# Performance work log

Hardware: AMD Instinct MI355X
Metric: run time of the kernel (lower is better)

The kernel has to match this reference:

```python
import jax, jax.numpy as jnp
import numpy as np

HID = 256
NCLASS = 5
DEPTH = 11          # complete binary tree, N = 2**DEPTH - 1 nodes
BATCH = 128
N_NODES = 2 ** DEPTH - 1


def setup_inputs() -> dict:
    key = jax.random.key(0)
    ks = jax.random.split(key, 16)
    scale = 0.1
    def mat(k, shape):
        return scale * jax.random.normal(k, shape, dtype=jnp.float32)
    inp = {
        "x": jax.random.normal(ks[0], (BATCH, N_NODES, HID), dtype=jnp.float32),
        "W_i": mat(ks[1], (HID, HID)),
        "U_i": mat(ks[2], (2, HID, HID)),
        "b_i": jnp.zeros((HID,), jnp.float32),
        "W_f": mat(ks[3], (HID, HID)),
        "U_f": mat(ks[4], (2, 2, HID, HID)),
        "b_f": jnp.zeros((HID,), jnp.float32),
        "W_o": mat(ks[5], (HID, HID)),
        "U_o": mat(ks[6], (2, HID, HID)),
        "b_o": jnp.zeros((HID,), jnp.float32),
        "W_u": mat(ks[7], (HID, HID)),
        "U_u": mat(ks[8], (2, HID, HID)),
        "b_u": jnp.zeros((HID,), jnp.float32),
        "W_s": mat(ks[9], (NCLASS, HID)),
        "b_s": jnp.zeros((NCLASS,), jnp.float32),
    }
    return inp


def _mv(W, v):
    # W: [h,h] (or [c,h]), v: [B,M,h] -> [B,M,h_out]; matches U.mul(h).sum(dim=1)
    return jnp.einsum('ij,bmj->bmi', W, v)


def _tree_lstm(x, W_i, U_i, b_i, W_f, U_f, b_f, W_o, U_o, b_o, W_u, U_u, b_u):
    B, N, h = x.shape
    D = int(round(np.log2(N + 1)))
    h_all = jnp.zeros_like(x)   # init_tree: node_h = zeros
    c_all = jnp.zeros_like(x)   # init_tree: cell   = zeros
    for lvl in range(D - 1, -1, -1):  # bottom-up over tree levels
        s = 2 ** lvl - 1
        e = 2 ** (lvl + 1) - 1
        M = e - s
        x_lvl = x[:, s:e]                      # [B,M,h]
        if lvl == D - 1:  # leaves: children states are the zero-initialized ones
            hL = hR = cL = cR = jnp.zeros((B, M, h), x.dtype)
        else:
            # children of node i=s+j are at e+2j (left) and e+2j+1 (right)
            hc = h_all[:, e:e + 2 * M].reshape(B, M, 2, h)
            cc = c_all[:, e:e + 2 * M].reshape(B, M, 2, h)
            hL, hR = hc[:, :, 0], hc[:, :, 1]
            cL, cR = cc[:, :, 0], cc[:, :, 1]
        i_g = jax.nn.sigmoid(_mv(W_i, x_lvl) + _mv(U_i[0], hL) + _mv(U_i[1], hR) + b_i)
        o_g = jax.nn.sigmoid(_mv(W_o, x_lvl) + _mv(U_o[0], hL) + _mv(U_o[1], hR) + b_o)
        u_g = jnp.tanh(_mv(W_u, x_lvl) + _mv(U_u[0], hL) + _mv(U_u[1], hR) + b_u)
        Wfx = _mv(W_f, x_lvl)
        f0 = jax.nn.sigmoid(Wfx + _mv(U_f[0, 0], hL) + _mv(U_f[0, 1], hR) + b_f)
        f1 = jax.nn.sigmoid(Wfx + _mv(U_f[1, 0], hL) + _mv(U_f[1, 1], hR) + b_f)
        c_lvl = i_g * u_g + f0 * cL + f1 * cR
        h_lvl = o_g * jnp.tanh(c_lvl)
        h_all = h_all.at[:, s:e].set(h_lvl)
        c_all = c_all.at[:, s:e].set(c_lvl)
    return h_all


def reference(x, W_i, U_i, b_i, W_f, U_f, b_f, W_o, U_o, b_o, W_u, U_u, b_u, W_s, b_s):
    h_all = _tree_lstm(x, W_i, U_i, b_i, W_f, U_f, b_f, W_o, U_o, b_o, W_u, U_u, b_u)
    # PredictUpTree (dropout omitted for the deterministic reference):
    logits = jnp.einsum('ch,bnh->bnc', W_s, h_all) + b_s   # [B,N,Nclass]
    return jax.nn.softmax(logits, axis=-1)
```

## Files before the change

kernel.cpp:

```cpp
#include <hip/hip_runtime.h>
#include <math.h>

#define HID 256
#define NCLASS 5
#define DEPTH 11
#define NB 128
#define NN 2047

typedef __attribute__((ext_vector_type(8))) short bf16x8_t;
typedef __attribute__((ext_vector_type(4))) float f32x4_t;

__device__ __forceinline__ float bf2f(unsigned short u) {
    return __uint_as_float(((unsigned)u) << 16);
}
__device__ __forceinline__ unsigned short f2bf(float f) {
    unsigned x = __float_as_uint(f);
    unsigned r = (x + 0x7fff + ((x >> 16) & 1)) >> 16;
    return (unsigned short)r;
}
__device__ __forceinline__ float sigmoidf_(float x) {
    return __fdividef(1.0f, 1.0f + __expf(-x));
}
__device__ __forceinline__ float tanhf_(float x) {
    return 1.0f - __fdividef(2.0f, __expf(2.0f * x) + 1.0f);
}
__device__ __forceinline__ void gl_lds16(const void* g, void* l) {
    __builtin_amdgcn_global_load_lds(
        (const __attribute__((address_space(1))) unsigned int*)g,
        (__attribute__((address_space(3))) unsigned int*)l,
        16, 0, 0);
}

__global__ __launch_bounds__(256)
void prep_wcat(const float* __restrict__ W_i, const float* __restrict__ U_i,
               const float* __restrict__ W_f, const float* __restrict__ U_f,
               const float* __restrict__ W_o, const float* __restrict__ U_o,
               const float* __restrict__ W_u, const float* __restrict__ U_u,
               unsigned short* __restrict__ Wcat)
{
    int idx = blockIdx.x * 256 + threadIdx.x;
    int k = idx % 768;
    int n = idx / 768;
    int g = n >> 8;
    int ch = n & 255;
    int seg = k >> 8;
    int kk = k & 255;
    float v;
    if (seg == 0) {
        const float* W = (g == 0) ? W_i : (g == 1) ? W_o : (g == 2) ? W_u : W_f;
        v = W[ch * 256 + kk];
    } else {
        int side = seg - 1;
        if (g == 0)      v = U_i[(side * 256 + ch) * 256 + kk];
        else if (g == 1) v = U_o[(side * 256 + ch) * 256 + kk];
        else if (g == 2) v = U_u[(side * 256 + ch) * 256 + kk];
        else             v = U_f[(((g - 3) * 2 + side) * 256 + ch) * 256 + kk];
    }
    Wcat[(size_t)n * 768 + k] = f2bf(v);
}

__global__ __launch_bounds__(256)
void cast_x_kernel(const float* __restrict__ x, unsigned short* __restrict__ xb)
{
    size_t i = ((size_t)blockIdx.x * 256 + threadIdx.x) * 8;
    float4 a = *(const float4*)(x + i);
    float4 b = *(const float4*)(x + i + 4);
    unsigned short o[8] = {f2bf(a.x), f2bf(a.y), f2bf(a.z), f2bf(a.w),
                           f2bf(b.x), f2bf(b.y), f2bf(b.z), f2bf(b.w)};
    *(uint4*)(xb + i) = *(uint4*)o;
}

template<int NG, int NK, bool LEAF>
__global__ __launch_bounds__(512, 4)
void level_gemm(const unsigned short* __restrict__ xb,
                const unsigned short* __restrict__ hA,
                const unsigned short* __restrict__ Wcat,
                const float* __restrict__ c_child,
                const float* __restrict__ b_i, const float* __restrict__ b_o,
                const float* __restrict__ b_u, const float* __restrict__ b_f,
                float* __restrict__ c_out,
                unsigned short* __restrict__ hA_parent,
                unsigned short* __restrict__ h_all,
                int lgM)
{
    constexpr int NT = NG * 4;
    constexpr int BOFF = 8192;
    constexpr int BUFSZ = BOFF + NT * 1024;
    __shared__ __align__(16) char smem[2 * BUFSZ];

    const int tid  = threadIdx.x;
    const int w    = tid >> 6, lane = tid & 63;
    const int quad = lane >> 4, p = lane & 15;
    const int rh = w & 1, cq = w >> 1;
    const int chblk = blockIdx.x;
    const int R0 = blockIdx.y * 128;
    const int M = 1 << lgM, s = M - 1;

    const int arow = R0 + w * 16 + p;
    const int ab = arow >> lgM, am = arow & (M - 1);
    const unsigned short* a_x = xb + ((size_t)ab * NN + s + am) * 256 + quad * 8;
    const unsigned short* a_h = LEAF ? (const unsigned short*)nullptr
                                     : hA + (size_t)arow * 512 + quad * 8;
    const int nbt = LEAF ? (w < 4 ? 2 : 1) : (w < 4 ? 3 : 2);
    const int t0  = LEAF ? (w < 4 ? w * 2 : 8 + (w - 4))
                         : (w < 4 ? w * 3 : 12 + (w - 4) * 2);
    const unsigned short* bsrc[3];
    #pragma unroll
    for (int j = 0; j < 3; ++j) {
        int t = t0 + ((j < nbt) ? j : 0);
        int n = (t >> 2) * 256 + chblk * 64 + (t & 3) * 16 + p;
        bsrc[j] = Wcat + (size_t)n * 768 + quad * 8;
    }

    f32x4_t acc[4][NG];
    #pragma unroll
    for (int mi = 0; mi < 4; ++mi)
        #pragma unroll
        for (int j = 0; j < NG; ++j)
            acc[mi][j] = (f32x4_t){0.f, 0.f, 0.f, 0.f};

    {
        gl_lds16(a_x, smem + w * 1024);
        #pragma unroll
        for (int j = 0; j < 3; ++j)
            if (j < nbt) gl_lds16(bsrc[j], smem + BOFF + (t0 + j) * 1024);
    }
    __syncthreads();

    for (int step = 0; step < NK; ++step) {
        char* bufc = smem + (size_t)(step & 1) * BUFSZ;
        if (step + 1 < NK) {
            char* bufn = smem + (size_t)((step + 1) & 1) * BUFSZ;
            const int k0 = (step + 1) * 32;
            const unsigned short* asrc = (LEAF || k0 < 256) ? (a_x + k0) : (a_h + (k0 - 256));
            gl_lds16(asrc, bufn + w * 1024);
            #pragma unroll
            for (int j = 0; j < 3; ++j)
                if (j < nbt) gl_lds16(bsrc[j] + k0, bufn + BOFF + (t0 + j) * 1024);
        }
        __builtin_amdgcn_sched_barrier(0);

        bf16x8_t af[4];
        #pragma unroll
        for (int mi = 0; mi < 4; ++mi)
            af[mi] = *(const bf16x8_t*)(bufc + ((rh * 4 + mi) * 64 + lane) * 16);
        __builtin_amdgcn_s_setprio(1);
        #pragma unroll
        for (int j = 0; j < NG; ++j) {
            bf16x8_t bfr = *(const bf16x8_t*)(bufc + BOFF + ((j * 4 + cq) * 64 + lane) * 16);
            #pragma unroll
            for (int mi = 0; mi < 4; ++mi)
                acc[mi][j] = __builtin_amdgcn_mfma_f32_16x16x32_bf16(af[mi], bfr, acc[mi][j], 0, 0, 0);
        }
        __builtin_amdgcn_s_setprio(0);
        __syncthreads();
    }

    const int gch = chblk * 64 + cq * 16 + p;
    const float bi = b_i[gch], bo = b_o[gch], bu = b_u[gch];
    const float bfv = LEAF ? 0.f : b_f[gch];

    #pragma unroll
    for (int mi = 0; mi < 4; ++mi) {
        const int rowq = R0 + rh * 64 + mi * 16 + quad * 4;
        #pragma unroll
        for (int reg = 0; reg < 4; ++reg) {
            const int grow = rowq + reg;
            const int b = grow >> lgM, m = grow & (M - 1);
            float ig = sigmoidf_(acc[mi][0][reg] + bi);
            float og = sigmoidf_(acc[mi][1][reg] + bo);
            float ug = tanhf_(acc[mi][2][reg] + bu);
            float c;
            if (LEAF) {
                c = ig * ug;
            } else {
                const float* crow = c_child + ((size_t)b * (M << 1) + 2 * m) * 256 + gch;
                float f0 = sigmoidf_(acc[mi][3][reg] + bfv);
                float f1 = sigmoidf_(acc[mi][4][reg] + bfv);
                c = fmaf(f0, crow[0], fmaf(f1, crow[256], ig * ug));
            }
            float h = og * tanhf_(c);
            c_out[(size_t)grow * 256 + gch] = c;
            unsigned short hb = f2bf(h);
            h_all[((size_t)b * NN + s + m) * 256 + gch] = hb;
            if (hA_parent)
                hA_parent[((size_t)b * (M >> 1) + (m >> 1)) * 512 + (m & 1) * 256 + gch] = hb;
        }
    }
}

__global__ __launch_bounds__(256)
void softmax_kernel(const unsigned short* __restrict__ h_all,
                    const float* __restrict__ W_s, const float* __restrict__ b_s,
                    float* __restrict__ out)
{
    __shared__ float Ws[5 * 256];
    int tid = threadIdx.x;
    for (int i = tid; i < 1280; i += 256) Ws[i] = W_s[i];
    __syncthreads();

    int r = tid >> 3, q = tid & 7;
    size_t row = (size_t)blockIdx.x * 32 + r;
    const unsigned short* hp = h_all + row * 256 + q * 32;

    float p0 = 0.f, p1 = 0.f, p2 = 0.f, p3 = 0.f, p4 = 0.f;
    #pragma unroll
    for (int kk = 0; kk < 32; kk += 8) {
        uint4 raw = *(const uint4*)(hp + kk);
        unsigned short hu[8];
        *(uint4*)hu = raw;
        #pragma unroll
        for (int e = 0; e < 8; ++e) {
            float hvv = bf2f(hu[e]);
            int k = q * 32 + kk + e;
            p0 = fmaf(Ws[k],        hvv, p0);
            p1 = fmaf(Ws[256 + k],  hvv, p1);
            p2 = fmaf(Ws[512 + k],  hvv, p2);
            p3 = fmaf(Ws[768 + k],  hvv, p3);
            p4 = fmaf(Ws[1024 + k], hvv, p4);
        }
    }
    #pragma unroll
    for (int off = 4; off; off >>= 1) {
        p0 += __shfl_down(p0, off, 8);
        p1 += __shfl_down(p1, off, 8);
        p2 += __shfl_down(p2, off, 8);
        p3 += __shfl_down(p3, off, 8);
        p4 += __shfl_down(p4, off, 8);
    }
    if (q == 0) {
        float l0 = p0 + b_s[0], l1 = p1 + b_s[1], l2 = p2 + b_s[2];
        float l3 = p3 + b_s[3], l4 = p4 + b_s[4];
        float mx = fmaxf(fmaxf(fmaxf(l0, l1), fmaxf(l2, l3)), l4);
        float e0 = __expf(l0 - mx), e1 = __expf(l1 - mx), e2 = __expf(l2 - mx);
        float e3 = __expf(l3 - mx), e4 = __expf(l4 - mx);
        float inv = 1.0f / (e0 + e1 + e2 + e3 + e4);
        float* orow = out + row * NCLASS;
        orow[0] = e0 * inv;
        orow[1] = e1 * inv;
        orow[2] = e2 * inv;
        orow[3] = e3 * inv;
        orow[4] = e4 * inv;
    }
}

extern "C" void kernel_launch(void* const* d_in, const int* in_sizes, int n_in,
                              void* d_out, int out_size, void* d_ws, size_t ws_size,
                              hipStream_t stream) {
    const float* x   = (const float*)d_in[0];
    const float* W_i = (const float*)d_in[1];
    const float* U_i = (const float*)d_in[2];
    const float* b_i = (const float*)d_in[3];
    const float* W_f = (const float*)d_in[4];
    const float* U_f = (const float*)d_in[5];
    const float* b_f = (const float*)d_in[6];
    const float* W_o = (const float*)d_in[7];
    const float* U_o = (const float*)d_in[8];
    const float* b_o = (const float*)d_in[9];
    const float* W_u = (const float*)d_in[10];
    const float* U_u = (const float*)d_in[11];
    const float* b_u = (const float*)d_in[12];
    const float* W_s = (const float*)d_in[13];
    const float* b_s = (const float*)d_in[14];
    float* out = (float*)d_out;

    char* p = (char*)d_ws;
    unsigned short* Wcat  = (unsigned short*)p; p += 2097152;
    unsigned short* xb    = (unsigned short*)p; p += 134152192;
    unsigned short* h_all = (unsigned short*)p; p += 134152192;
    unsigned short* hA0   = (unsigned short*)p; p += 33554432;
    unsigned short* hA1   = (unsigned short*)p; p += 67108864;
    float* cb0 = (float*)p; p += 134217728;
    float* cb1 = (float*)p; p += 67108864;

    prep_wcat<<<3840, 256, 0, stream>>>(W_i, U_i, W_f, U_f, W_o, U_o, W_u, U_u, Wcat);
    cast_x_kernel<<<32752, 256, 0, stream>>>(x, xb);

    for (int lvl = DEPTH - 1; lvl >= 0; --lvl) {
        dim3 grid(4, 1 << lvl);
        float* c_o        = (lvl & 1) ? cb1 : cb0;
        const float* c_ch = ((lvl + 1) & 1) ? cb1 : cb0;
        const unsigned short* hA_this = (lvl & 1) ? hA1 : hA0;
        unsigned short* hA_par = (lvl > 0) ? (((lvl - 1) & 1) ? hA1 : hA0) : nullptr;

        if (lvl == DEPTH - 1) {
            level_gemm<3, 8, true><<<grid, 512, 0, stream>>>(
                xb, nullptr, Wcat, nullptr, b_i, b_o, b_u, b_f,
                c_o, hA_par, h_all, lvl);
        } else {
            level_gemm<5, 24, false><<<grid, 512, 0, stream>>>(
                xb, hA_this, Wcat, c_ch, b_i, b_o, b_u, b_f,
                c_o, hA_par, h_all, lvl);
        }
    }

    softmax_kernel<<<8188, 256, 0, stream>>>(h_all, W_s, b_s, out);
}
```

Before: 1.299 ms.

## Replace LDS-staged GEMM with direct global-to-register double buffering and block swizzle

```diff
diff --git a/kernel.cpp b/kernel.cpp
--- a/kernel.cpp
+++ b/kernel.cpp
@@ -23,12 +23,6 @@
 }
 __device__ __forceinline__ float tanhf_(float x) {
     return 1.0f - __fdividef(2.0f, __expf(2.0f * x) + 1.0f);
-}
-__device__ __forceinline__ void gl_lds16(const void* g, void* l) {
-    __builtin_amdgcn_global_load_lds(
-        (const __attribute__((address_space(1))) unsigned int*)g,
-        (__attribute__((address_space(3))) unsigned int*)l,
-        16, 0, 0);
 }
 
 __global__ __launch_bounds__(256)
@@ -71,7 +65,7 @@
 }
 
 template<int NG, int NK, bool LEAF>
-__global__ __launch_bounds__(512, 4)
+__global__ __launch_bounds__(512, LEAF ? 3 : 2)
 void level_gemm(const unsigned short* __restrict__ xb,
                 const unsigned short* __restrict__ hA,
                 const unsigned short* __restrict__ Wcat,
@@ -81,35 +75,43 @@
                 float* __restrict__ c_out,
                 unsigned short* __restrict__ hA_parent,
                 unsigned short* __restrict__ h_all,
-                int lgM)
+                int lgM, int nrb)
 {
-    constexpr int NT = NG * 4;
-    constexpr int BOFF = 8192;
-    constexpr int BUFSZ = BOFF + NT * 1024;
-    __shared__ __align__(16) char smem[2 * BUFSZ];
-
     const int tid  = threadIdx.x;
-    const int w    = tid >> 6, lane = tid & 63;
+    const int lane = tid & 63;
+    const int w    = tid >> 6;
     const int quad = lane >> 4, p = lane & 15;
     const int rh = w & 1, cq = w >> 1;
-    const int chblk = blockIdx.x;
-    const int R0 = blockIdx.y * 128;
+
+    int chblk, rb;
+    {
+        int bid = blockIdx.x;
+        if ((nrb & 7) == 0) {
+            int x = bid & 7, sl = bid >> 3;
+            chblk = sl & 3;
+            rb = x + 8 * (sl >> 2);
+        } else {
+            chblk = bid & 3;
+            rb = bid >> 2;
+        }
+    }
+    const int R0 = rb * 128;
     const int M = 1 << lgM, s = M - 1;
 
-    const int arow = R0 + w * 16 + p;
-    const int ab = arow >> lgM, am = arow & (M - 1);
-    const unsigned short* a_x = xb + ((size_t)ab * NN + s + am) * 256 + quad * 8;
-    const unsigned short* a_h = LEAF ? (const unsigned short*)nullptr
-                                     : hA + (size_t)arow * 512 + quad * 8;
-    const int nbt = LEAF ? (w < 4 ? 2 : 1) : (w < 4 ? 3 : 2);
-    const int t0  = LEAF ? (w < 4 ? w * 2 : 8 + (w - 4))
-                         : (w < 4 ? w * 3 : 12 + (w - 4) * 2);
-    const unsigned short* bsrc[3];
-    #pragma unroll
-    for (int j = 0; j < 3; ++j) {
-        int t = t0 + ((j < nbt) ? j : 0);
-        int n = (t >> 2) * 256 + chblk * 64 + (t & 3) * 16 + p;
-        bsrc[j] = Wcat + (size_t)n * 768 + quad * 8;
+    const unsigned short* ax[4];
+    const unsigned short* ah[4];
+    #pragma unroll
+    for (int mi = 0; mi < 4; ++mi) {
+        const int arow = R0 + (rh * 4 + mi) * 16 + p;
+        const int ab = arow >> lgM, am = arow & (M - 1);
+        ax[mi] = xb + ((size_t)ab * NN + s + am) * 256 + quad * 8;
+        ah[mi] = LEAF ? ax[mi] : hA + (size_t)arow * 512 + quad * 8;
+    }
+    const unsigned short* bb[NG];
+    #pragma unroll
+    for (int j = 0; j < NG; ++j) {
+        int n = j * 256 + chblk * 64 + cq * 16 + p;
+        bb[j] = Wcat + (size_t)n * 768 + quad * 8;
     }
 
     f32x4_t acc[4][NG];
@@ -119,42 +121,41 @@
         for (int j = 0; j < NG; ++j)
             acc[mi][j] = (f32x4_t){0.f, 0.f, 0.f, 0.f};
 
-    {
-        gl_lds16(a_x, smem + w * 1024);
-        #pragma unroll
-        for (int j = 0; j < 3; ++j)
-            if (j < nbt) gl_lds16(bsrc[j], smem + BOFF + (t0 + j) * 1024);
-    }
-    __syncthreads();
-
-    for (int step = 0; step < NK; ++step) {
-        char* bufc = smem + (size_t)(step & 1) * BUFSZ;
-        if (step + 1 < NK) {
-            char* bufn = smem + (size_t)((step + 1) & 1) * BUFSZ;
-            const int k0 = (step + 1) * 32;
-            const unsigned short* asrc = (LEAF || k0 < 256) ? (a_x + k0) : (a_h + (k0 - 256));
-            gl_lds16(asrc, bufn + w * 1024);
-            #pragma unroll
-            for (int j = 0; j < 3; ++j)
-                if (j < nbt) gl_lds16(bsrc[j] + k0, bufn + BOFF + (t0 + j) * 1024);
-        }
-        __builtin_amdgcn_sched_barrier(0);
-
-        bf16x8_t af[4];
-        #pragma unroll
-        for (int mi = 0; mi < 4; ++mi)
-            af[mi] = *(const bf16x8_t*)(bufc + ((rh * 4 + mi) * 64 + lane) * 16);
-        __builtin_amdgcn_s_setprio(1);
-        #pragma unroll
-        for (int j = 0; j < NG; ++j) {
-            bf16x8_t bfr = *(const bf16x8_t*)(bufc + BOFF + ((j * 4 + cq) * 64 + lane) * 16);
-            #pragma unroll
-            for (int mi = 0; mi < 4; ++mi)
-                acc[mi][j] = __builtin_amdgcn_mfma_f32_16x16x32_bf16(af[mi], bfr, acc[mi][j], 0, 0, 0);
-        }
-        __builtin_amdgcn_s_setprio(0);
-        __syncthreads();
-    }
+    bf16x8_t fa0[4], fa1[4];
+    bf16x8_t fb0[NG], fb1[NG];
+
+    #define LOAD_A(k0, fa)                                                        \
+        _Pragma("unroll")                                                         \
+        for (int mi = 0; mi < 4; ++mi) {                                          \
+            const unsigned short* srcA = (LEAF || (k0) < 256) ? (ax[mi] + (k0))   \
+                                                  : (ah[mi] + ((k0) - 256));      \
+            fa[mi] = *(const bf16x8_t*)srcA;                                      \
+        }
+    #define LOAD_B(k0, fb)                                                        \
+        _Pragma("unroll")                                                         \
+        for (int j = 0; j < NG; ++j)                                              \
+            fb[j] = *(const bf16x8_t*)(bb[j] + (k0));
+    #define COMPUTE(fa, fb)                                                       \
+        _Pragma("unroll")                                                         \
+        for (int j = 0; j < NG; ++j)                                              \
+            _Pragma("unroll")                                                     \
+            for (int mi = 0; mi < 4; ++mi)                                        \
+                acc[mi][j] = __builtin_amdgcn_mfma_f32_16x16x32_bf16(             \
+                    fa[mi], fb[j], acc[mi][j], 0, 0, 0);
+
+    LOAD_A(0, fa0); LOAD_B(0, fb0);
+    LOAD_A(32, fa1); LOAD_B(32, fb1);
+
+    #pragma unroll
+    for (int st = 0; st < NK; st += 2) {
+        COMPUTE(fa0, fb0);
+        if (st + 2 < NK) { LOAD_A((st + 2) * 32, fa0); LOAD_B((st + 2) * 32, fb0); }
+        COMPUTE(fa1, fb1);
+        if (st + 3 < NK) { LOAD_A((st + 3) * 32, fa1); LOAD_B((st + 3) * 32, fb1); }
+    }
+    #undef LOAD_A
+    #undef LOAD_B
+    #undef COMPUTE
 
     const int gch = chblk * 64 + cq * 16 + p;
     const float bi = b_i[gch], bo = b_o[gch], bu = b_u[gch];
@@ -163,6 +164,17 @@
     #pragma unroll
     for (int mi = 0; mi < 4; ++mi) {
         const int rowq = R0 + rh * 64 + mi * 16 + quad * 4;
+        float cl[4], cr[4];
+        if (!LEAF) {
+            #pragma unroll
+            for (int reg = 0; reg < 4; ++reg) {
+                const int grow = rowq + reg;
+                const int b = grow >> lgM, m = grow & (M - 1);
+                const float* crow = c_child + ((size_t)b * (M << 1) + 2 * m) * 256 + gch;
+                cl[reg] = crow[0];
+                cr[reg] = crow[256];
+            }
+        }
         #pragma unroll
         for (int reg = 0; reg < 4; ++reg) {
             const int grow = rowq + reg;
@@ -174,10 +186,9 @@
             if (LEAF) {
                 c = ig * ug;
             } else {
-                const float* crow = c_child + ((size_t)b * (M << 1) + 2 * m) * 256 + gch;
                 float f0 = sigmoidf_(acc[mi][3][reg] + bfv);
                 float f1 = sigmoidf_(acc[mi][4][reg] + bfv);
-                c = fmaf(f0, crow[0], fmaf(f1, crow[256], ig * ug));
+                c = fmaf(f0, cl[reg], fmaf(f1, cr[reg], ig * ug));
             }
             float h = og * tanhf_(c);
             c_out[(size_t)grow * 256 + gch] = c;
@@ -277,20 +288,20 @@
     cast_x_kernel<<<32752, 256, 0, stream>>>(x, xb);
 
     for (int lvl = DEPTH - 1; lvl >= 0; --lvl) {
-        dim3 grid(4, 1 << lvl);
         float* c_o        = (lvl & 1) ? cb1 : cb0;
         const float* c_ch = ((lvl + 1) & 1) ? cb1 : cb0;
         const unsigned short* hA_this = (lvl & 1) ? hA1 : hA0;
         unsigned short* hA_par = (lvl > 0) ? (((lvl - 1) & 1) ? hA1 : hA0) : nullptr;
 
+        const int nrb = 1 << lvl;
         if (lvl == DEPTH - 1) {
-            level_gemm<3, 8, true><<<grid, 512, 0, stream>>>(
+            level_gemm<3, 8, true><<<dim3(4 * nrb), 512, 0, stream>>>(
                 xb, nullptr, Wcat, nullptr, b_i, b_o, b_u, b_f,
-                c_o, hA_par, h_all, lvl);
+                c_o, hA_par, h_all, lvl, nrb);
         } else {
-            level_gemm<5, 24, false><<<grid, 512, 0, stream>>>(
+            level_gemm<5, 24, false><<<dim3(4 * nrb), 512, 0, stream>>>(
                 xb, hA_this, Wcat, c_ch, b_i, b_o, b_u, b_f,
-                c_o, hA_par, h_all, lvl);
+                c_o, hA_par, h_all, lvl, nrb);
         }
     }
 
```

Result: slower. 1.875 ms (+44.4%).
